# Optimization experiments

Measured on AMD Instinct MI355X. Metric: run time of the kernel, lower is better.

Reference implementation:

```python
import jax, jax.numpy as jnp
import numpy as np

B, L, H, V = 256, 200, 128, 50000
NLAYER, K = 2, 20
NEG = -1e10


def setup_inputs() -> dict:
    key = jax.random.key(0)
    ks = jax.random.split(key, 14)
    lens = jax.random.randint(ks[0], (B,), 50, L + 1)
    pos = jnp.arange(L)
    valid = pos[None, :] < lens[:, None]                       # [B,L] bool
    seq = jnp.where(valid, jax.random.randint(ks[1], (B, L), 1, V), 0)
    lengths = valid.astype(jnp.int32)                          # >0 where real token
    reverse_lengths = jnp.where(valid, lens[:, None] - pos[None, :], 0)  # 1..len, 0=pad

    def nrm(k, shape, s=0.02):
        return jax.random.normal(k, shape, jnp.float32) * s

    emb_w = nrm(ks[2], (V, H)).at[0].set(0.0)
    wnoise_w = nrm(ks[3], (L + 1, H)).at[0].set(0.0)
    cluster_w = nrm(ks[4], (L + 1, 1)).at[0].set(0.0)
    ffn1_w = nrm(ks[5], (H, H), 0.05)
    ffn1_b = jnp.zeros((H,), jnp.float32)
    ffn2_w = nrm(ks[6], (H, H), 0.05)
    ffn2_b = jnp.zeros((H,), jnp.float32)
    ln_g = jnp.ones((H,), jnp.float32)
    ln_b = jnp.zeros((H,), jnp.float32)
    gate_w = nrm(ks[7], (2 * H, H), 0.05)
    coff = jax.random.normal(ks[8], (NLAYER, B, L, L), jnp.float32)  # fixed noise (torch.normal)
    return dict(seq=seq, lengths=lengths, reverse_lengths=reverse_lengths,
                emb_w=emb_w, wnoise_w=wnoise_w, cluster_w=cluster_w,
                ffn1_w=ffn1_w, ffn1_b=ffn1_b, ffn2_w=ffn2_w, ffn2_b=ffn2_b,
                ln_g=ln_g, ln_b=ln_b, gate_w=gate_w, coff=coff)


def _sp(x):  # torch.nn.Softplus(threshold=1): identity above 1
    return jnp.where(x > 1.0, x, jnp.log1p(jnp.exp(jnp.minimum(x, 1.0))))


def _forward(seq, lengths, reverse_lengths, emb_w, wnoise_w, cluster_w,
             ffn1_w, ffn1_b, ffn2_w, ffn2_b, ln_g, ln_b, gate_w, coff):
    b, l = seq.shape
    mask = (lengths > 0).astype(jnp.float32)                   # [B,L]
    hidden = emb_w[seq]                                        # [B,L,H]
    slen = jnp.sum(mask, axis=1)                               # [B]
    e_s = hidden[jnp.arange(b), (slen - 1).astype(jnp.int32)]  # last real token state
    zero_layer = jnp.sum(hidden, 1) / slen[:, None]
    layer_collect = [zero_layer]
    eye = jnp.eye(l, dtype=hidden.dtype)
    pair_ok = mask[:, :, None] * mask[:, None, :]              # [B,L,L]
    for i in range(coff.shape[0]):
        wn = wnoise_w[reverse_lengths]                         # [B,L,H]
        sim = jnp.einsum('bld,bmd->blm', hidden, hidden)
        nrm = jnp.linalg.norm(hidden, axis=2, keepdims=True)   # [B,L,1]
        sim = sim / (nrm * nrm.transpose(0, 2, 1) + 1e-6)      # cosine similarity
        diag = cluster_w[reverse_lengths][..., 0]              # [B,L]
        sim = sim + diag[:, :, None] * eye                     # diag_embed add
        sim = sim + coff[i] * _sp(jnp.einsum('bld,bmd->blm', hidden, wn))
        msim = jnp.where(pair_ok == 0.0, NEG, sim)             # masked_fill
        _, idx = jax.lax.top_k(msim, K)                        # [B,L,K]
        sel = jnp.zeros_like(msim).at[jnp.arange(b)[:, None, None],
                                      jnp.arange(l)[None, :, None], idx].set(1.0)
        edges = sel * (msim > NEG).astype(msim.dtype)          # top-k & above-threshold
        cluster_label = edges.transpose(0, 2, 1)
        sim_softmax = jax.nn.softmax(msim, axis=2)
        ssm = cluster_label * sim_softmax                      # [B,L,L] sparse-weighted
        update_hidden = jnp.einsum('blm,bmd->bld', ssm, hidden)
        cmask = jnp.sum(ssm, axis=2)                           # [B,L]
        cmask = cmask / jnp.maximum(jnp.linalg.norm(cmask, axis=1, keepdims=True), 1e-12)
        if i > 0:
            update_hidden = update_hidden * (slen > 1.0).astype(hidden.dtype)[:, None, None]
        feed1 = jax.nn.relu(update_hidden @ ffn1_w + ffn1_b)
        pre = feed1 @ ffn2_w + ffn2_b + update_hidden          # dropout = identity (eval)
        mu = jnp.mean(pre, -1, keepdims=True)
        var = jnp.var(pre, -1, keepdims=True)
        feed2 = (pre - mu) / jnp.sqrt(var + 1e-5) * ln_g + ln_b
        layer_collect.append(jnp.sum(feed2 * cmask[:, :, None], 1))
    e_c = jnp.mean(jnp.stack(layer_collect, 1), 1)             # [B,H]
    alpha = jax.nn.sigmoid(jnp.concatenate([e_c, e_s], -1) @ gate_w)
    sess = alpha * e_c + (1.0 - alpha) * e_s
    scores = sess @ emb_w.T                                    # [B,V]
    return scores


def reference(seq, lengths, reverse_lengths, emb_w, wnoise_w, cluster_w,
              ffn1_w, ffn1_b, ffn2_w, ffn2_b, ln_g, ln_b, gate_w, coff):
    scores = _forward(seq, lengths, reverse_lengths, emb_w, wnoise_w, cluster_w,
                      ffn1_w, ffn1_b, ffn2_w, ffn2_b, ln_g, ln_b, gate_w, coff)
    return (scores, jnp.asarray(0.0, jnp.float32))  # con_loss == 0 when abs=True
```

## Files before the change

### kernel.cpp

```cpp
#include <hip/hip_runtime.h>
#include <cstdint>
#include <cstddef>

namespace {
constexpr int B = 256, L = 200, H = 128, V = 50000, TK = 20;
constexpr float NEGV = -1e10f;
}

using bf16x8 = __attribute__((ext_vector_type(8))) short;
using s16x8  = __attribute__((ext_vector_type(8))) short;
using f32x16 = __attribute__((ext_vector_type(16))) float;

__device__ inline unsigned short f2bf(float f) {
  unsigned int u = __float_as_uint(f);
  unsigned int r = (u + 0x7fffu + ((u >> 16) & 1u)) >> 16;
  return (unsigned short)r;
}

#define DPP_QUAD_XOR1 0xB1
#define DPP_QUAD_XOR2 0x4E
#define DPP_ROW_HMIRR 0x141
#define DPP_ROW_MIRR  0x140

template <int CTRL>
__device__ inline unsigned dpp16_max_step(unsigned v) {
  unsigned t = (unsigned)__builtin_amdgcn_update_dpp(0, (int)v, CTRL, 0xF, 0xF, true);
  return v > t ? v : t;
}
__device__ inline unsigned grp16_max(unsigned v) {
  v = dpp16_max_step<DPP_QUAD_XOR1>(v);
  v = dpp16_max_step<DPP_QUAD_XOR2>(v);
  v = dpp16_max_step<DPP_ROW_HMIRR>(v);
  v = dpp16_max_step<DPP_ROW_MIRR>(v);
  return v;
}
template <int CTRL>
__device__ inline float dpp16_add_step(float v) {
  int t = __builtin_amdgcn_update_dpp(0, __float_as_int(v), CTRL, 0xF, 0xF, true);
  return v + __int_as_float(t);
}
__device__ inline float grp16_sum(float v) {
  v = dpp16_add_step<DPP_QUAD_XOR1>(v);
  v = dpp16_add_step<DPP_QUAD_XOR2>(v);
  v = dpp16_add_step<DPP_ROW_HMIRR>(v);
  v = dpp16_add_step<DPP_ROW_MIRR>(v);
  return v;
}

__device__ inline unsigned f2key(float f) {
  unsigned b = __float_as_uint(f);
  unsigned m = (unsigned)((int)b >> 31);
  return b ^ (m | 0x80000000u);
}
__device__ inline float key2f(unsigned u) {
  unsigned b = (u & 0x80000000u) ? (u & 0x7fffffffu) : ~u;
  return __uint_as_float(b);
}

__global__ __launch_bounds__(256) void k_embed(const int* __restrict__ seq,
                                               const int* __restrict__ rev,
                                               const float* __restrict__ emb,
                                               const float* __restrict__ wnoise,
                                               float* __restrict__ hidden,
                                               float* __restrict__ nrm,
                                               s16x8* __restrict__ hbh,
                                               s16x8* __restrict__ hbl,
                                               s16x8* __restrict__ wnh,
                                               s16x8* __restrict__ wnl) {
  int b = blockIdx.x / 7, lt = blockIdx.x % 7;
  int t = threadIdx.x;
  int r = t >> 3, c2 = t & 7;
  int l = lt * 32 + r;
  bool valid = l < L;
  float vv[16], wv[16];
  if (valid) {
    int row = b * L + l;
    int tok = seq[row];
    const float4* ep = (const float4*)&emb[(size_t)tok * H + c2 * 16];
    const float4* wp = (const float4*)&wnoise[(size_t)rev[row] * H + c2 * 16];
#pragma unroll
    for (int i = 0; i < 4; ++i) {
      float4 x = ep[i];
      vv[i * 4 + 0] = x.x; vv[i * 4 + 1] = x.y; vv[i * 4 + 2] = x.z; vv[i * 4 + 3] = x.w;
      float4 y = wp[i];
      wv[i * 4 + 0] = y.x; wv[i * 4 + 1] = y.y; wv[i * 4 + 2] = y.z; wv[i * 4 + 3] = y.w;
    }
  } else {
#pragma unroll
    for (int i = 0; i < 16; ++i) { vv[i] = 0.f; wv[i] = 0.f; }
  }
  if (valid) {
    int row = b * L + l;
#pragma unroll
    for (int i = 0; i < 4; ++i)
      *(float4*)&hidden[(size_t)row * H + c2 * 16 + i * 4] =
          make_float4(vv[i * 4], vv[i * 4 + 1], vv[i * 4 + 2], vv[i * 4 + 3]);
    float s = 0.f;
#pragma unroll
    for (int i = 0; i < 16; ++i) s += vv[i] * vv[i];
    s += __shfl_down(s, 4, 8);
    s += __shfl_down(s, 2, 8);
    s += __shfl_down(s, 1, 8);
    if (c2 == 0) nrm[row] = sqrtf(s);
  }
  s16x8 h0, h1, l0, l1, w0, w1, x0, x1;
#pragma unroll
  for (int i = 0; i < 8; ++i) {
    unsigned short hi = f2bf(vv[i]);
    h0[i] = (short)hi;
    l0[i] = (short)f2bf(vv[i] - __uint_as_float((unsigned)hi << 16));
    unsigned short wh = f2bf(wv[i]);
    w0[i] = (short)wh;
    x0[i] = (short)f2bf(wv[i] - __uint_as_float((unsigned)wh << 16));
  }
#pragma unroll
  for (int i = 0; i < 8; ++i) {
    unsigned short hi = f2bf(vv[8 + i]);
    h1[i] = (short)hi;
    l1[i] = (short)f2bf(vv[8 + i] - __uint_as_float((unsigned)hi << 16));
    unsigned short wh = f2bf(wv[8 + i]);
    w1[i] = (short)wh;
    x1[i] = (short)f2bf(wv[8 + i] - __uint_as_float((unsigned)wh << 16));
  }
  size_t fi0 = ((size_t)(b * 7 + lt) * 8 + c2) * 64 + r;
  size_t fi1 = fi0 + 32;
  hbh[fi0] = h0; hbh[fi1] = h1;
  hbl[fi0] = l0; hbl[fi1] = l1;
  wnh[fi0] = w0; wnh[fi1] = w1;
  wnl[fi0] = x0; wnl[fi1] = x1;
}

__global__ __launch_bounds__(512) void k_init(const int* __restrict__ lengths,
                                              const float* __restrict__ hidden,
                                              float* __restrict__ ecacc,
                                              float* __restrict__ e_s) {
  int b = blockIdx.x, tid = threadIdx.x;
  __shared__ float part[4][128];
  __shared__ int wcnt[8];
  __shared__ int s_slen;
  int c = (tid < L && lengths[b * L + tid] > 0) ? 1 : 0;
  for (int o = 32; o > 0; o >>= 1) c += __shfl_down(c, o, 64);
  if ((tid & 63) == 0) wcnt[tid >> 6] = c;
  __syncthreads();
  if (tid == 0) {
    int s = 0;
#pragma unroll
    for (int i = 0; i < 8; ++i) s += wcnt[i];
    s_slen = s;
  }
  int h = tid & 127, seg = tid >> 7;
  float s = 0.f;
  for (int l = seg; l < L; l += 4) s += hidden[(size_t)(b * L + l) * H + h];
  part[seg][h] = s;
  __syncthreads();
  if (tid < 128) {
    float tot = part[0][h] + part[1][h] + part[2][h] + part[3][h];
    int slen = s_slen;
    ecacc[b * H + h] = tot / (float)slen;
    e_s[b * H + h] = hidden[(size_t)(b * L + slen - 1) * H + h];
  }
}

__global__ __launch_bounds__(256) void k_simws(const s16x8* __restrict__ hbh,
                                               const s16x8* __restrict__ hbl,
                                               const s16x8* __restrict__ wnh,
                                               const s16x8* __restrict__ wnl,
                                               const float* __restrict__ nrm,
                                               const int* __restrict__ rev,
                                               const float* __restrict__ cluster,
                                               float* __restrict__ S0,
                                               float* __restrict__ WS) {
  int orig = blockIdx.x;
  int xcd = orig & 7, slot = orig >> 3;
  int b = xcd * 32 + slot / 7, lt = slot % 7;
  int wid = threadIdx.x >> 6, lane = threadIdx.x & 63;
  int lr = lane & 31, kh = lane >> 5;
  size_t abase = ((size_t)(b * 7 + lt) * 8) * 64 + lane;
  bf16x8 ah[8], al[8];
#pragma unroll
  for (int ks = 0; ks < 8; ++ks) {
    ah[ks] = (bf16x8)hbh[abase + ks * 64];
    al[ks] = (bf16x8)hbl[abase + ks * 64];
  }
  for (int mt = wid; mt < 7; mt += 4) {
    size_t bbase = ((size_t)(b * 7 + mt) * 8) * 64 + lane;
    f32x16 accs = {}, accw = {};
#pragma unroll
    for (int ks = 0; ks < 8; ++ks) {
      bf16x8 bhh = (bf16x8)hbh[bbase + ks * 64];
      bf16x8 bhl = (bf16x8)hbl[bbase + ks * 64];
      bf16x8 bwh = (bf16x8)wnh[bbase + ks * 64];
      bf16x8 bwl = (bf16x8)wnl[bbase + ks * 64];
      accs = __builtin_amdgcn_mfma_f32_32x32x16_bf16(ah[ks], bhh, accs, 0, 0, 0);
      accs = __builtin_amdgcn_mfma_f32_32x32x16_bf16(ah[ks], bhl, accs, 0, 0, 0);
      accs = __builtin_amdgcn_mfma_f32_32x32x16_bf16(al[ks], bhh, accs, 0, 0, 0);
      accw = __builtin_amdgcn_mfma_f32_32x32x16_bf16(ah[ks], bwh, accw, 0, 0, 0);
      accw = __builtin_amdgcn_mfma_f32_32x32x16_bf16(ah[ks], bwl, accw, 0, 0, 0);
      accw = __builtin_amdgcn_mfma_f32_32x32x16_bf16(al[ks], bwh, accw, 0, 0, 0);
    }
    int m = mt * 32 + lr;
    if (m < L) {
      float nm = nrm[b * L + m];
#pragma unroll
      for (int r = 0; r < 16; ++r) {
        int row = lt * 32 + (r & 3) + 8 * (r >> 2) + 4 * kh;
        if (row < L) {
          float nl = nrm[b * L + row];
          float s0 = accs[r] * __builtin_amdgcn_rcpf(nl * nm + 1e-6f);
          if (row == m) s0 += cluster[rev[b * L + row]];
          size_t o = (size_t)(b * L + row) * L + m;
          S0[o] = s0;
          float x = accw[r];
          WS[o] = (x > 1.f) ? x : __logf(1.f + __expf(x));
        }
      }
    }
  }
}

__global__ __launch_bounds__(256) void k_rowpass(const float* __restrict__ S0,
                                                 const float* __restrict__ WS,
                                                 const float* __restrict__ coff_i,
                                                 const int* __restrict__ lengths,
                                                 float* __restrict__ P,
                                                 unsigned char* __restrict__ ET) {
  int wid = threadIdx.x >> 6, lane = threadIdx.x & 63;
  int g = lane >> 4, q = lane & 15;
  int bb = blockIdx.x / 13, blk = blockIdx.x % 13;
  int l = blk * 16 + wid * 4 + g;
  bool lvalid = l < L;
  int lrow = bb * L + (lvalid ? l : 0);
  bool mask_l = lvalid && (lengths[lrow] > 0);
  size_t base = (size_t)lrow * L;
  float val[13]; unsigned key[13]; unsigned vmask = 0;
#pragma unroll
  for (int j = 0; j < 13; ++j) {
    int m = q + 16 * j;
    float v = 0.f; bool ok = false;
    if (mask_l && m < L) {
      ok = lengths[bb * L + m] > 0;
      if (ok) v = S0[base + m] + coff_i[base + m] * WS[base + m];
    }
    val[j] = v;
    key[j] = ok ? f2key(v) : 0u;
    vmask |= ok ? (1u << j) : 0u;
  }
  unsigned Mu = 0u;
  for (int t = 0; t < TK; ++t) {
    unsigned lv = key[0]; int lj = 0;
#pragma unroll
    for (int j = 1; j < 13; ++j) {
      bool gt = key[j] > lv;
      lv = gt ? key[j] : lv;
      lj = gt ? j : lj;
    }
    unsigned gm = grp16_max(lv);
    if (t == 0) Mu = gm;
    if (__all(gm == 0u)) break;
    unsigned long long bal = __ballot(lv == gm && gm != 0u);
    unsigned long long mine = bal & (0xFFFFull << (g * 16));
    int owner = mine ? (int)__builtin_ctzll(mine) : -1;
    bool is_owner = (lane == owner);
    if (is_owner) {
      int m = q + 16 * lj;
      ET[((size_t)bb * L + m) * L + l] = 1;
    }
#pragma unroll
    for (int j = 0; j < 13; ++j) key[j] = (is_owner && lj == j) ? 0u : key[j];
  }
  float M = key2f(Mu);
  float e[13]; float s = 0.f;
#pragma unroll
  for (int j = 0; j < 13; ++j) {
    float ev = ((vmask >> j) & 1u) ? __expf(val[j] - M) : 0.f;
    e[j] = ev; s += ev;
  }
  s = grp16_sum(s);
  float inv = (s > 0.f) ? __builtin_amdgcn_rcpf(s) : 0.f;
  if (lvalid) {
#pragma unroll
    for (int j = 0; j < 13; ++j) {
      int m = q + 16 * j;
      if (m < L) P[base + m] = e[j] * inv;
    }
  }
}

__global__ __launch_bounds__(256) void k_compact(float* __restrict__ P,
                                                 unsigned char* __restrict__ ET,
                                                 float* __restrict__ cmask,
                                                 int* __restrict__ cnt) {
  int wid = threadIdx.x >> 6, lane = threadIdx.x & 63;
  int row = blockIdx.x * 4 + wid;
  size_t base = (size_t)row * L;
  float w[4];
  float s = 0.f;
#pragma unroll
  for (int j = 0; j < 4; ++j) {
    int m = lane + 64 * j;
    float ww = 0.f;
    if (m < L) ww = P[base + m] * (float)ET[base + m];
    w[j] = ww; s += ww;
  }
  float ssum = s;
  for (int off = 1; off < 64; off <<= 1) ssum += __shfl_xor(ssum, off, 64);
  if (lane == 0) cmask[row] = ssum;
  int pos_base = 0;
#pragma unroll
  for (int j = 0; j < 4; ++j) {
    bool nz = (w[j] != 0.f);
    unsigned long long mk = __ballot(nz);
    int rank = __popcll(mk & ((1ull << lane) - 1ull));
    if (nz) {
      int pos = pos_base + rank;
      ET[base + pos] = (unsigned char)(lane + 64 * j);
      P[base + pos] = w[j];
    }
    pos_base += (int)__popcll(mk);
  }
  if (lane == 0) cnt[row] = pos_base;
}

__global__ __launch_bounds__(64) void k_cnorm(float* __restrict__ cmask) {
  int b = blockIdx.x, lane = threadIdx.x;
  float v[4]; float s = 0.f;
#pragma unroll
  for (int j = 0; j < 4; ++j) {
    int l = lane + 64 * j;
    float x = (l < L) ? cmask[b * L + l] : 0.f;
    v[j] = x; s += x * x;
  }
  for (int off = 1; off < 64; off <<= 1) s += __shfl_xor(s, off, 64);
  float inv = 1.f / fmaxf(sqrtf(s), 1e-12f);
#pragma unroll
  for (int j = 0; j < 4; ++j) {
    int l = lane + 64 * j;
    if (l < L) cmask[b * L + l] = v[j] * inv;
  }
}

__global__ __launch_bounds__(256) void k_update(const float* __restrict__ P,
                                                const unsigned char* __restrict__ ET,
                                                const int* __restrict__ cnt,
                                                const float* __restrict__ hidden,
                                                float* __restrict__ upd) {
  int row = blockIdx.x * 2 + (threadIdx.x >> 7);
  int h = threadIdx.x & 127;
  int b = row / L;
  size_t base = (size_t)row * L;
  int n = cnt[row];
  float acc = 0.f;
  for (int e0 = 0; e0 < n; e0 += TK) {
    float w[TK]; int m[TK];
    float4 p4[5];
#pragma unroll
    for (int i = 0; i < 5; ++i) p4[i] = *(const float4*)&P[base + e0 + i * 4];
#pragma unroll
    for (int i = 0; i < 5; ++i) {
      w[i * 4 + 0] = p4[i].x; w[i * 4 + 1] = p4[i].y;
      w[i * 4 + 2] = p4[i].z; w[i * 4 + 3] = p4[i].w;
    }
#pragma unroll
    for (int e = 0; e < TK; ++e) m[e] = ET[base + e0 + e];
    float hv[TK];
#pragma unroll
    for (int e = 0; e < TK; ++e)
      hv[e] = hidden[(size_t)(b * L + m[e]) * H + h];
#pragma unroll
    for (int e = 0; e < TK; ++e)
      acc += ((e0 + e) < n ? w[e] : 0.f) * hv[e];
  }
  upd[(size_t)row * H + h] = acc;
}

__global__ __launch_bounds__(256) void k_ffn(float* __restrict__ upd,
                                             const float* __restrict__ W1,
                                             const float* __restrict__ b1,
                                             const float* __restrict__ W2,
                                             const float* __restrict__ b2,
                                             const float* __restrict__ g,
                                             const float* __restrict__ beta,
                                             const float* __restrict__ cmask) {
  constexpr int AS = 136;
  __shared__ __align__(16) char smem[4 * 64 * AS * 2];
  short* ahs = (short*)smem;
  short* als = ahs + 64 * AS;
  short* f1h = (short*)(smem + 2 * 64 * AS * 2);
  short* f1l = f1h + 64 * AS;
  float (*ps)[132] = (float (*)[132])smem;
  __shared__ float mus[64], rsd[64];
  int row0 = blockIdx.x * 64;
  int tid = threadIdx.x;
  int wid = tid >> 6, lane = tid & 63;
  int lr = lane & 31, kh = lane >> 5;
  int n0 = wid * 32;
  int n = n0 + lr;
#pragma unroll
  for (int it = 0; it < 8; ++it) {
    int f = it * 256 + tid;
    int r = f >> 5, c4 = (f & 31) * 4;
    float4 v = *(const float4*)&upd[(size_t)(row0 + r) * H + c4];
    float vv[4] = {v.x, v.y, v.z, v.w};
    unsigned short hh[4]; short ll[4];
#pragma unroll
    for (int q2 = 0; q2 < 4; ++q2) {
      hh[q2] = f2bf(vv[q2]);
      ll[q2] = (short)f2bf(vv[q2] - __uint_as_float((unsigned)hh[q2] << 16));
    }
    uint2 ph = make_uint2((unsigned)hh[0] | ((unsigned)hh[1] << 16),
                          (unsigned)hh[2] | ((unsigned)hh[3] << 16));
    uint2 pl = make_uint2((unsigned short)ll[0] | ((unsigned)(unsigned short)ll[1] << 16),
                          (unsigned short)ll[2] | ((unsigned)(unsigned short)ll[3] << 16));
    *(uint2*)&ahs[r * AS + c4] = ph;
    *(uint2*)&als[r * AS + c4] = pl;
  }
  __syncthreads();
  bf16x8 wfh[8], wfl[8];
#pragma unroll
  for (int ks = 0; ks < 8; ++ks) {
#pragma unroll
    for (int i = 0; i < 8; ++i) {
      float w = W1[(size_t)(ks * 16 + kh * 8 + i) * H + n];
      unsigned short hi = f2bf(w);
      wfh[ks][i] = (short)hi;
      wfl[ks][i] = (short)f2bf(w - __uint_as_float((unsigned)hi << 16));
    }
  }
  f32x16 acc0, acc1;
  {
    float bv = b1[n];
#pragma unroll
    for (int r = 0; r < 16; ++r) { acc0[r] = bv; acc1[r] = bv; }
  }
#pragma unroll
  for (int ks = 0; ks < 8; ++ks) {
    bf16x8 xh0 = *(const bf16x8*)&ahs[(0 * 32 + lr) * AS + ks * 16 + kh * 8];
    bf16x8 xl0 = *(const bf16x8*)&als[(0 * 32 + lr) * AS + ks * 16 + kh * 8];
    bf16x8 xh1 = *(const bf16x8*)&ahs[(1 * 32 + lr) * AS + ks * 16 + kh * 8];
    bf16x8 xl1 = *(const bf16x8*)&als[(1 * 32 + lr) * AS + ks * 16 + kh * 8];
    acc0 = __builtin_amdgcn_mfma_f32_32x32x16_bf16(xh0, wfh[ks], acc0, 0, 0, 0);
    acc0 = __builtin_amdgcn_mfma_f32_32x32x16_bf16(xl0, wfh[ks], acc0, 0, 0, 0);
    acc0 = __builtin_amdgcn_mfma_f32_32x32x16_bf16(xh0, wfl[ks], acc0, 0, 0, 0);
    acc1 = __builtin_amdgcn_mfma_f32_32x32x16_bf16(xh1, wfh[ks], acc1, 0, 0, 0);
    acc1 = __builtin_amdgcn_mfma_f32_32x32x16_bf16(xl1, wfh[ks], acc1, 0, 0, 0);
    acc1 = __builtin_amdgcn_mfma_f32_32x32x16_bf16(xh1, wfl[ks], acc1, 0, 0, 0);
  }
#pragma unroll
  for (int r = 0; r < 16; ++r) {
    int crow = (r & 3) + 8 * (r >> 2) + 4 * kh;
    float f0 = fmaxf(acc0[r], 0.f);
    unsigned short h0 = f2bf(f0);
    f1h[crow * AS + n] = (short)h0;
    f1l[crow * AS + n] = (short)f2bf(f0 - __uint_as_float((unsigned)h0 << 16));
    float f1v = fmaxf(acc1[r], 0.f);
    unsigned short h1 = f2bf(f1v);
    f1h[(32 + crow) * AS + n] = (short)h1;
    f1l[(32 + crow) * AS + n] = (short)f2bf(f1v - __uint_as_float((unsigned)h1 << 16));
  }
  __syncthreads();
#pragma unroll
  for (int ks = 0; ks < 8; ++ks) {
#pragma unroll
    for (int i = 0; i < 8; ++i) {
      float w = W2[(size_t)(ks * 16 + kh * 8 + i) * H + n];
      unsigned short hi = f2bf(w);
      wfh[ks][i] = (short)hi;
      wfl[ks][i] = (short)f2bf(w - __uint_as_float((unsigned)hi << 16));
    }
  }
  {
    float bv = b2[n];
#pragma unroll
    for (int r = 0; r < 16; ++r) { acc0[r] = bv; acc1[r] = bv; }
  }
#pragma unroll
  for (int ks = 0; ks < 8; ++ks) {
    bf16x8 xh0 = *(const bf16x8*)&f1h[(0 * 32 + lr) * AS + ks * 16 + kh * 8];
    bf16x8 xl0 = *(const bf16x8*)&f1l[(0 * 32 + lr) * AS + ks * 16 + kh * 8];
    bf16x8 xh1 = *(const bf16x8*)&f1h[(1 * 32 + lr) * AS + ks * 16 + kh * 8];
    bf16x8 xl1 = *(const bf16x8*)&f1l[(1 * 32 + lr) * AS + ks * 16 + kh * 8];
    acc0 = __builtin_amdgcn_mfma_f32_32x32x16_bf16(xh0, wfh[ks], acc0, 0, 0, 0);
    acc0 = __builtin_amdgcn_mfma_f32_32x32x16_bf16(xl0, wfh[ks], acc0, 0, 0, 0);
    acc0 = __builtin_amdgcn_mfma_f32_32x32x16_bf16(xh0, wfl[ks], acc0, 0, 0, 0);
    acc1 = __builtin_amdgcn_mfma_f32_32x32x16_bf16(xh1, wfh[ks], acc1, 0, 0, 0);
    acc1 = __builtin_amdgcn_mfma_f32_32x32x16_bf16(xl1, wfh[ks], acc1, 0, 0, 0);
    acc1 = __builtin_amdgcn_mfma_f32_32x32x16_bf16(xh1, wfl[ks], acc1, 0, 0, 0);
  }
#pragma unroll
  for (int r = 0; r < 16; ++r) {
    int crow = (r & 3) + 8 * (r >> 2) + 4 * kh;
    float p0 = acc0[r] + upd[(size_t)(row0 + crow) * H + n];
    float p1 = acc1[r] + upd[(size_t)(row0 + 32 + crow) * H + n];
    acc0[r] = p0; acc1[r] = p1;
    ps[crow][n] = p0;
    ps[32 + crow][n] = p1;
  }
  __syncthreads();
  {
    int r = tid >> 2, sub = tid & 3;
    float s = 0.f, sq = 0.f;
#pragma unroll
    for (int j = 0; j < 8; ++j) {
      float4 x = *(const float4*)&ps[r][sub * 32 + j * 4];
      s += x.x + x.y + x.z + x.w;
      sq += x.x * x.x + x.y * x.y + x.z * x.z + x.w * x.w;
    }
    s += __shfl_down(s, 2, 4);  s += __shfl_down(s, 1, 4);
    sq += __shfl_down(sq, 2, 4); sq += __shfl_down(sq, 1, 4);
    if (sub == 0) {
      float mu = s * (1.f / 128.f);
      float var = sq * (1.f / 128.f) - mu * mu;
      mus[r] = mu;
      rsd[r] = rsqrtf(var + 1e-5f);
    }
  }
  __syncthreads();
  {
    float gn = g[n], bn = beta[n];
#pragma unroll
    for (int r = 0; r < 16; ++r) {
      int crow = (r & 3) + 8 * (r >> 2) + 4 * kh;
      float o0 = ((acc0[r] - mus[crow]) * rsd[crow] * gn + bn) * cmask[row0 + crow];
      float o1 = ((acc1[r] - mus[32 + crow]) * rsd[32 + crow] * gn + bn) * cmask[row0 + 32 + crow];
      upd[(size_t)(row0 + crow) * H + n] = o0;
      upd[(size_t)(row0 + 32 + crow) * H + n] = o1;
    }
  }
}

__global__ __launch_bounds__(512) void k_ecadd(const float* __restrict__ wf,
                                               float* __restrict__ ecacc) {
  int b = blockIdx.x, tid = threadIdx.x;
  __shared__ float part[4][128];
  int h = tid & 127, seg = tid >> 7;
  float s = 0.f;
  for (int l = seg; l < L; l += 4) s += wf[(size_t)(b * L + l) * H + h];
  part[seg][h] = s;
  __syncthreads();
  if (tid < 128)
    ecacc[b * H + h] += part[0][h] + part[1][h] + part[2][h] + part[3][h];
}

__global__ __launch_bounds__(128) void k_gate(const float* __restrict__ ecacc,
                                              const float* __restrict__ e_s,
                                              const float* __restrict__ gw,
                                              float* __restrict__ sess,
                                              float* __restrict__ out) {
  __shared__ float cat[256];
  int b = blockIdx.x, h = threadIdx.x;
  float ec = ecacc[b * H + h] * (1.f / 3.f);
  float es = e_s[b * H + h];
  cat[h] = ec; cat[128 + h] = es;
  __syncthreads();
  float a = 0.f;
  for (int j = 0; j < 256; ++j) a = fmaf(cat[j], gw[(size_t)j * H + h], a);
  a = 1.f / (1.f + __expf(-a));
  sess[b * H + h] = a * ec + (1.f - a) * es;
  if (b == 0 && h == 0) out[(size_t)B * V] = 0.f;
}

__global__ __launch_bounds__(256) void k_scores(const float* __restrict__ sess,
                                                const float* __restrict__ emb,
                                                float* __restrict__ out) {
  __shared__ float As[64][65], Bs[64][65];
  int n0 = blockIdx.x * 64, m0 = blockIdx.y * 64;
  int tid = threadIdx.x, tx = tid & 15, ty = tid >> 4;
  int tx4 = tx * 4, ty4 = ty * 4;
  float acc[4][4] = {};
  for (int kc = 0; kc < H; kc += 64) {
#pragma unroll
    for (int it = 0; it < 4; ++it) {
      int r = it * 16 + ty, c4 = tx4;
      float4 av = *(const float4*)&sess[(size_t)(m0 + r) * H + kc + c4];
      As[r][c4 + 0] = av.x; As[r][c4 + 1] = av.y; As[r][c4 + 2] = av.z; As[r][c4 + 3] = av.w;
      float4 bv = make_float4(0.f, 0.f, 0.f, 0.f);
      if (n0 + r < V) bv = *(const float4*)&emb[(size_t)(n0 + r) * H + kc + c4];
      Bs[r][c4 + 0] = bv.x; Bs[r][c4 + 1] = bv.y; Bs[r][c4 + 2] = bv.z; Bs[r][c4 + 3] = bv.w;
    }
    __syncthreads();
#pragma unroll 8
    for (int kk = 0; kk < 64; ++kk) {
      float a[4], bb[4];
#pragma unroll
      for (int i = 0; i < 4; ++i) a[i] = As[ty4 + i][kk];
#pragma unroll
      for (int j = 0; j < 4; ++j) bb[j] = Bs[tx4 + j][kk];
#pragma unroll
      for (int i = 0; i < 4; ++i)
#pragma unroll
        for (int j = 0; j < 4; ++j) acc[i][j] = fmaf(a[i], bb[j], acc[i][j]);
    }
    __syncthreads();
  }
#pragma unroll
  for (int i = 0; i < 4; ++i) {
    int m = m0 + ty4 + i;
#pragma unroll
    for (int j = 0; j < 4; ++j) {
      int n = n0 + tx4 + j;
      if (n < V) out[(size_t)m * V + n] = acc[i][j];
    }
  }
}

extern "C" void kernel_launch(void* const* d_in, const int* in_sizes, int n_in,
                              void* d_out, int out_size, void* d_ws, size_t ws_size,
                              hipStream_t stream) {
  const int*   seq  = (const int*)d_in[0];
  const int*   lens = (const int*)d_in[1];
  const int*   rev  = (const int*)d_in[2];
  const float* emb  = (const float*)d_in[3];
  const float* wnz  = (const float*)d_in[4];
  const float* clw  = (const float*)d_in[5];
  const float* w1   = (const float*)d_in[6];
  const float* fb1  = (const float*)d_in[7];
  const float* w2   = (const float*)d_in[8];
  const float* fb2  = (const float*)d_in[9];
  const float* lng  = (const float*)d_in[10];
  const float* lnb  = (const float*)d_in[11];
  const float* gw   = (const float*)d_in[12];
  const float* coff = (const float*)d_in[13];
  float* out = (float*)d_out;

  char* ws = (char*)d_ws;
  size_t off = 0;
  auto alloc = [&](size_t bytes) {
    void* p = ws + off;
    off += (bytes + 255) & ~(size_t)255;
    return p;
  };
  float* hidden = (float*)alloc((size_t)B * L * H * 4);
  float* nrm    = (float*)alloc((size_t)B * L * 4);
  float* S0     = (float*)alloc((size_t)B * L * L * 4);
  float* WS     = (float*)alloc((size_t)B * L * L * 4);
  float* P      = (float*)alloc((size_t)B * L * L * 4);
  float* upd    = (float*)alloc((size_t)B * L * H * 4);
  float* cmask  = (float*)alloc((size_t)B * L * 4);
  int*   cnt    = (int*)alloc((size_t)B * L * 4);
  float* e_s    = (float*)alloc((size_t)B * H * 4);
  float* ecacc  = (float*)alloc((size_t)B * H * 4);
  float* sess   = (float*)alloc((size_t)B * H * 4);
  unsigned char* ET = (unsigned char*)alloc((size_t)B * L * L);
  s16x8* hbh = (s16x8*)alloc((size_t)B * 7 * 8 * 64 * 16);
  s16x8* wnh = (s16x8*)alloc((size_t)B * 7 * 8 * 64 * 16);
  s16x8* hbl = (s16x8*)P;
  s16x8* wnl = (s16x8*)upd;

  k_embed<<<B * 7, 256, 0, stream>>>(seq, rev, emb, wnz, hidden, nrm,
                                     hbh, hbl, wnh, wnl);
  k_init<<<B, 512, 0, stream>>>(lens, hidden, ecacc, e_s);
  k_simws<<<B * 7, 256, 0, stream>>>(hbh, hbl, wnh, wnl, nrm, rev, clw, S0, WS);

  for (int i = 0; i < 2; ++i) {
    hipMemsetAsync(ET, 0, (size_t)B * L * L, stream);
    k_rowpass<<<B * 13, 256, 0, stream>>>(S0, WS, coff + (size_t)i * B * L * L,
                                          lens, P, ET);
    k_compact<<<B * L / 4, 256, 0, stream>>>(P, ET, cmask, cnt);
    k_cnorm<<<B, 64, 0, stream>>>(cmask);
    k_update<<<B * L / 2, 256, 0, stream>>>(P, ET, cnt, hidden, upd);
    k_ffn<<<B * L / 64, 256, 0, stream>>>(upd, w1, fb1, w2, fb2, lng, lnb, cmask);
    k_ecadd<<<B, 512, 0, stream>>>(upd, ecacc);
  }

  k_gate<<<B, 128, 0, stream>>>(ecacc, e_s, gw, sess, out);
  k_scores<<<dim3((V + 63) / 64, 4), 256, 0, stream>>>(sess, emb, out);
}
```

Before: 494.3 us.

## Compute final scores GEMM with split-bf16 MFMA using pre-swizzled embedding table

Replaces the FP32 LDS-tiled SIMT GEMM for scores = sess @ emb^T with MFMA 32x32x16 bf16 instructions. Both operands are split into hi/lo bf16 parts and multiplied three times to keep close to fp32 accuracy. A new pre-pass kernel converts the embedding table into hi/lo bf16 in an MFMA-friendly fragment layout, reusing dead scratch buffers. The cost is an extra full pass over the embedding table plus triple MFMA work, and the output stores are strided rather than coalesced.

```diff
diff --git a/kernel.cpp b/kernel.cpp
--- a/kernel.cpp
+++ b/kernel.cpp
@@ -4,6 +4,7 @@
 
 namespace {
 constexpr int B = 256, L = 200, H = 128, V = 50000, TK = 20;
+constexpr int NT = 1563;
 constexpr float NEGV = -1e10f;
 }
 
@@ -541,6 +542,41 @@
     ecacc[b * H + h] += part[0][h] + part[1][h] + part[2][h] + part[3][h];
 }
 
+__global__ __launch_bounds__(256) void k_embconv(const float* __restrict__ emb,
+                                                 s16x8* __restrict__ ebh,
+                                                 s16x8* __restrict__ ebl) {
+  int nt = blockIdx.x;
+  int t = threadIdx.x;
+  int r = t >> 3, c2 = t & 7;
+  int n = nt * 32 + r;
+  float vv[16];
+  if (n < V) {
+    const float4* ep = (const float4*)&emb[(size_t)n * H + c2 * 16];
+#pragma unroll
+    for (int i = 0; i < 4; ++i) {
+      float4 x = ep[i];
+      vv[i * 4 + 0] = x.x; vv[i * 4 + 1] = x.y; vv[i * 4 + 2] = x.z; vv[i * 4 + 3] = x.w;
+    }
+  } else {
+#pragma unroll
+    for (int i = 0; i < 16; ++i) vv[i] = 0.f;
+  }
+  s16x8 h0, h1, l0, l1;
+#pragma unroll
+  for (int i = 0; i < 8; ++i) {
+    unsigned short hi = f2bf(vv[i]);
+    h0[i] = (short)hi;
+    l0[i] = (short)f2bf(vv[i] - __uint_as_float((unsigned)hi << 16));
+    unsigned short hj = f2bf(vv[8 + i]);
+    h1[i] = (short)hj;
+    l1[i] = (short)f2bf(vv[8 + i] - __uint_as_float((unsigned)hj << 16));
+  }
+  size_t fi0 = ((size_t)nt * 8 + c2) * 64 + r;
+  size_t fi1 = fi0 + 32;
+  ebh[fi0] = h0; ebh[fi1] = h1;
+  ebl[fi0] = l0; ebl[fi1] = l1;
+}
+
 __global__ __launch_bounds__(128) void k_gate(const float* __restrict__ ecacc,
                                               const float* __restrict__ e_s,
                                               const float* __restrict__ gw,
@@ -560,45 +596,46 @@
 }
 
 __global__ __launch_bounds__(256) void k_scores(const float* __restrict__ sess,
-                                                const float* __restrict__ emb,
+                                                const s16x8* __restrict__ ebh,
+                                                const s16x8* __restrict__ ebl,
                                                 float* __restrict__ out) {
-  __shared__ float As[64][65], Bs[64][65];
-  int n0 = blockIdx.x * 64, m0 = blockIdx.y * 64;
-  int tid = threadIdx.x, tx = tid & 15, ty = tid >> 4;
-  int tx4 = tx * 4, ty4 = ty * 4;
-  float acc[4][4] = {};
-  for (int kc = 0; kc < H; kc += 64) {
-#pragma unroll
-    for (int it = 0; it < 4; ++it) {
-      int r = it * 16 + ty, c4 = tx4;
-      float4 av = *(const float4*)&sess[(size_t)(m0 + r) * H + kc + c4];
-      As[r][c4 + 0] = av.x; As[r][c4 + 1] = av.y; As[r][c4 + 2] = av.z; As[r][c4 + 3] = av.w;
-      float4 bv = make_float4(0.f, 0.f, 0.f, 0.f);
-      if (n0 + r < V) bv = *(const float4*)&emb[(size_t)(n0 + r) * H + kc + c4];
-      Bs[r][c4 + 0] = bv.x; Bs[r][c4 + 1] = bv.y; Bs[r][c4 + 2] = bv.z; Bs[r][c4 + 3] = bv.w;
-    }
-    __syncthreads();
-#pragma unroll 8
-    for (int kk = 0; kk < 64; ++kk) {
-      float a[4], bb[4];
-#pragma unroll
-      for (int i = 0; i < 4; ++i) a[i] = As[ty4 + i][kk];
-#pragma unroll
-      for (int j = 0; j < 4; ++j) bb[j] = Bs[tx4 + j][kk];
-#pragma unroll
-      for (int i = 0; i < 4; ++i)
-#pragma unroll
-        for (int j = 0; j < 4; ++j) acc[i][j] = fmaf(a[i], bb[j], acc[i][j]);
-    }
-    __syncthreads();
-  }
-#pragma unroll
-  for (int i = 0; i < 4; ++i) {
-    int m = m0 + ty4 + i;
-#pragma unroll
-    for (int j = 0; j < 4; ++j) {
-      int n = n0 + tx4 + j;
-      if (n < V) out[(size_t)m * V + n] = acc[i][j];
+  int wid = threadIdx.x >> 6, lane = threadIdx.x & 63;
+  int lr = lane & 31, kh = lane >> 5;
+  int mt = blockIdx.y;
+  int m = mt * 32 + lr;
+  bf16x8 ah[8], al[8];
+#pragma unroll
+  for (int ks = 0; ks < 8; ++ks) {
+    const float* sp = &sess[(size_t)m * H + ks * 16 + kh * 8];
+    float4 a = *(const float4*)sp;
+    float4 c = *(const float4*)(sp + 4);
+    float av[8] = {a.x, a.y, a.z, a.w, c.x, c.y, c.z, c.w};
+#pragma unroll
+    for (int i = 0; i < 8; ++i) {
+      unsigned short hi = f2bf(av[i]);
+      ah[ks][i] = (short)hi;
+      al[ks][i] = (short)f2bf(av[i] - __uint_as_float((unsigned)hi << 16));
+    }
+  }
+  int ntEnd = min(blockIdx.x * 16 + 16, NT);
+  for (int nt = blockIdx.x * 16 + wid; nt < ntEnd; nt += 4) {
+    size_t bbase = ((size_t)nt * 8) * 64 + lane;
+    f32x16 acc = {};
+#pragma unroll
+    for (int ks = 0; ks < 8; ++ks) {
+      bf16x8 bh = (bf16x8)ebh[bbase + ks * 64];
+      bf16x8 bl = (bf16x8)ebl[bbase + ks * 64];
+      acc = __builtin_amdgcn_mfma_f32_32x32x16_bf16(ah[ks], bh, acc, 0, 0, 0);
+      acc = __builtin_amdgcn_mfma_f32_32x32x16_bf16(al[ks], bh, acc, 0, 0, 0);
+      acc = __builtin_amdgcn_mfma_f32_32x32x16_bf16(ah[ks], bl, acc, 0, 0, 0);
+    }
+    int n = nt * 32 + lr;
+    if (n < V) {
+#pragma unroll
+      for (int r = 0; r < 16; ++r) {
+        int row = mt * 32 + (r & 3) + 8 * (r >> 2) + 4 * kh;
+        out[(size_t)row * V + n] = acc[r];
+      }
     }
   }
 }
@@ -645,6 +682,8 @@
   s16x8* wnh = (s16x8*)alloc((size_t)B * 7 * 8 * 64 * 16);
   s16x8* hbl = (s16x8*)P;
   s16x8* wnl = (s16x8*)upd;
+  s16x8* ebh = (s16x8*)S0;
+  s16x8* ebl = (s16x8*)WS;
 
   k_embed<<<B * 7, 256, 0, stream>>>(seq, rev, emb, wnz, hidden, nrm,
                                      hbh, hbl, wnh, wnl);
@@ -662,6 +701,7 @@
     k_ecadd<<<B, 512, 0, stream>>>(upd, ecacc);
   }
 
+  k_embconv<<<NT, 256, 0, stream>>>(emb, ebh, ebl);
   k_gate<<<B, 128, 0, stream>>>(ecacc, e_s, gw, sess, out);
-  k_scores<<<dim3((V + 63) / 64, 4), 256, 0, stream>>>(sess, emb, out);
-}
+  k_scores<<<dim3((NT + 15) / 16, 8), 256, 0, stream>>>(sess, ebh, ebl, out);
+}
```

New measurement: 475.3 us. 3.9% less time.
